# Performance work log

Hardware: AMD Instinct MI355X
Metric: run time of the kernel (lower is better)

The kernel has to match this reference:

```python
import jax, jax.numpy as jnp
import numpy as np

def setup_inputs() -> dict:
    key = jax.random.key(0)
    inputs_embeds = jax.random.normal(key, (16, 8192, 256), dtype=jnp.float32)
    return {"inputs_embeds": inputs_embeds}

def reference(inputs_embeds):
    # cumulative prefix mean along seq dim: mean over [:i+1] = cumsum / (i+1)
    S = inputs_embeds.shape[1]
    csum = jnp.cumsum(inputs_embeds, axis=1)  # [B, S, D]
    denom = jnp.arange(1, S + 1, dtype=inputs_embeds.dtype)[None, :, None]
    return (csum / denom,)
```

## Files before the change

kernel.cpp:

```cpp
#include <hip/hip_runtime.h>

#define BB 16
#define SS 8192
#define DD 256
#define D4 (DD / 4)
#define NC 256
#define CL (SS / NC)
#define G  16

#define NBLK (BB * NC)
#define AGGA_OFF (64 * 1024)
#define AGG_BYTES (NBLK * DD * 4)
#define AGGI_OFF (AGGA_OFF + AGG_BYTES)
#define WS_NEEDED ((size_t)(AGGI_OFF + AGG_BYTES))

typedef float nat4 __attribute__((ext_vector_type(4)));

union F2U { float2 f; unsigned long long u; };

__global__ __launch_bounds__(256) void avgseq_init(int* __restrict__ flags) {
    const int i = blockIdx.x * 256 + threadIdx.x;
    if (i < NBLK) flags[i] = 0;
}

__global__ __launch_bounds__(64, 4) void avgseq_lookback(
    const float4* __restrict__ x, float4* __restrict__ out,
    int* __restrict__ flags, unsigned long long* __restrict__ aggA,
    unsigned long long* __restrict__ aggI)
{
    const int blk = blockIdx.x;
    const int b = blk >> 8;
    const int c = blk & (NC - 1);
    const int t = threadIdx.x;

    const size_t base = ((size_t)b * SS + (size_t)c * CL) * D4 + t;
    const float4* p = x + base;

    float4 agg = make_float4(0.f, 0.f, 0.f, 0.f);
    for (int s0 = 0; s0 < CL; s0 += G) {
        float4 v[G];
#pragma unroll
        for (int g = 0; g < G; ++g) v[g] = p[(size_t)(s0 + g) * D4];
#pragma unroll
        for (int g = 0; g < G; ++g) {
            agg.x += v[g].x; agg.y += v[g].y; agg.z += v[g].z; agg.w += v[g].w;
        }
    }

    const size_t slot = (size_t)blk * (DD / 2) + (size_t)t * 2;

    if (c > 0) {
        F2U lo, hi;
        lo.f = make_float2(agg.x, agg.y);
        hi.f = make_float2(agg.z, agg.w);
        __hip_atomic_store(&aggA[slot],     lo.u, __ATOMIC_RELAXED, __HIP_MEMORY_SCOPE_AGENT);
        __hip_atomic_store(&aggA[slot + 1], hi.u, __ATOMIC_RELAXED, __HIP_MEMORY_SCOPE_AGENT);
        asm volatile("s_waitcnt vmcnt(0)" ::: "memory");
        __hip_atomic_store(&flags[blk], 1, __ATOMIC_RELAXED, __HIP_MEMORY_SCOPE_AGENT);
    }

    double rx = 0.0, ry = 0.0, rz = 0.0, rw = 0.0;
    if (c > 0) {
        int cc = c - 1;
        for (;;) {
            const int fblk = (b << 8) + cc;
            int f;
            for (;;) {
                f = __hip_atomic_load(&flags[fblk], __ATOMIC_RELAXED, __HIP_MEMORY_SCOPE_AGENT);
                f = __builtin_amdgcn_readfirstlane(f);
                if (f != 0) break;
                __builtin_amdgcn_s_sleep(1);
            }
            const unsigned long long* src = (f == 2) ? aggI : aggA;
            const size_t s2 = (size_t)fblk * (DD / 2) + (size_t)t * 2;
            F2U a, bq;
            a.u  = __hip_atomic_load(&src[s2],     __ATOMIC_RELAXED, __HIP_MEMORY_SCOPE_AGENT);
            bq.u = __hip_atomic_load(&src[s2 + 1], __ATOMIC_RELAXED, __HIP_MEMORY_SCOPE_AGENT);
            rx += a.f.x; ry += a.f.y; rz += bq.f.x; rw += bq.f.y;
            if (f == 2) break;
            --cc;
        }
    }
    const float4 run = make_float4((float)rx, (float)ry, (float)rz, (float)rw);

    if (c < NC - 1) {
        F2U lo, hi;
        lo.f = make_float2(run.x + agg.x, run.y + agg.y);
        hi.f = make_float2(run.z + agg.z, run.w + agg.w);
        __hip_atomic_store(&aggI[slot],     lo.u, __ATOMIC_RELAXED, __HIP_MEMORY_SCOPE_AGENT);
        __hip_atomic_store(&aggI[slot + 1], hi.u, __ATOMIC_RELAXED, __HIP_MEMORY_SCOPE_AGENT);
        asm volatile("s_waitcnt vmcnt(0)" ::: "memory");
        __hip_atomic_store(&flags[blk], 2, __ATOMIC_RELAXED, __HIP_MEMORY_SCOPE_AGENT);
    }

    float4 acc = run;
    float4* o = out + base;
    const int sb = c * CL;
    for (int s0 = 0; s0 < CL; s0 += G) {
        float4 v[G];
#pragma unroll
        for (int g = 0; g < G; ++g) v[g] = p[(size_t)(s0 + g) * D4];
#pragma unroll
        for (int g = 0; g < G; ++g) {
            acc.x += v[g].x; acc.y += v[g].y; acc.z += v[g].z; acc.w += v[g].w;
            const float r = __builtin_amdgcn_rcpf((float)(sb + s0 + g + 1));
            v[g] = make_float4(acc.x * r, acc.y * r, acc.z * r, acc.w * r);
        }
#pragma unroll
        for (int g = 0; g < G; ++g) {
            nat4 nv = { v[g].x, v[g].y, v[g].z, v[g].w };
            __builtin_nontemporal_store(nv, (nat4*)&o[(size_t)(s0 + g) * D4]);
        }
    }
}

__global__ __launch_bounds__(64) void avgseq_chunksum(const float4* __restrict__ x,
                                                      float4* __restrict__ ws) {
    const int blk = blockIdx.x;
    const int b = blk >> 8;
    const int c = blk & (NC - 1);
    const int t = threadIdx.x;
    const float4* p = x + ((size_t)b * SS + (size_t)c * CL) * D4 + t;
    float4 acc = make_float4(0.f, 0.f, 0.f, 0.f);
    for (int s0 = 0; s0 < CL; s0 += G) {
        float4 v[G];
#pragma unroll
        for (int g = 0; g < G; ++g) v[g] = p[(size_t)(s0 + g) * D4];
#pragma unroll
        for (int g = 0; g < G; ++g) {
            acc.x += v[g].x; acc.y += v[g].y; acc.z += v[g].z; acc.w += v[g].w;
        }
    }
    ws[((size_t)b * NC + c) * D4 + t] = acc;
}

__global__ __launch_bounds__(64) void avgseq_scanws(float4* __restrict__ ws) {
    const int b = blockIdx.x;
    const int t = threadIdx.x;
    float4* w = ws + (size_t)b * NC * D4 + t;
    float4 run = make_float4(0.f, 0.f, 0.f, 0.f);
#pragma unroll 8
    for (int c = 0; c < NC; ++c) {
        float4 v = w[(size_t)c * D4];
        w[(size_t)c * D4] = run;
        run.x += v.x; run.y += v.y; run.z += v.z; run.w += v.w;
    }
}

__global__ __launch_bounds__(64) void avgseq_scan(const float4* __restrict__ x,
                                                  const float4* __restrict__ ws,
                                                  float4* __restrict__ out) {
    const int blk = blockIdx.x;
    const int b = blk >> 8;
    const int c = blk & (NC - 1);
    const int t = threadIdx.x;
    float4 acc = ws[((size_t)b * NC + c) * D4 + t];
    const size_t base = ((size_t)b * SS + (size_t)c * CL) * D4 + t;
    const float4* p = x + base;
    float4* o = out + base;
    const int s0 = c * CL;
    for (int ss = 0; ss < CL; ss += G) {
        float4 v[G];
#pragma unroll
        for (int g = 0; g < G; ++g) v[g] = p[(size_t)(ss + g) * D4];
#pragma unroll
        for (int g = 0; g < G; ++g) {
            acc.x += v[g].x; acc.y += v[g].y; acc.z += v[g].z; acc.w += v[g].w;
            const float r = __builtin_amdgcn_rcpf((float)(s0 + ss + g + 1));
            v[g] = make_float4(acc.x * r, acc.y * r, acc.z * r, acc.w * r);
        }
#pragma unroll
        for (int g = 0; g < G; ++g) o[(size_t)(ss + g) * D4] = v[g];
    }
}

extern "C" void kernel_launch(void* const* d_in, const int* in_sizes, int n_in,
                              void* d_out, int out_size, void* d_ws, size_t ws_size,
                              hipStream_t stream) {
    const float4* x = (const float4*)d_in[0];
    float4* out = (float4*)d_out;

    if (ws_size >= WS_NEEDED) {
        int* flags = (int*)d_ws;
        unsigned long long* aggA = (unsigned long long*)((char*)d_ws + AGGA_OFF);
        unsigned long long* aggI = (unsigned long long*)((char*)d_ws + AGGI_OFF);
        avgseq_init<<<(NBLK + 255) / 256, 256, 0, stream>>>(flags);
        avgseq_lookback<<<NBLK, 64, 0, stream>>>(x, out, flags, aggA, aggI);
    } else {
        float4* ws = (float4*)d_ws;
        avgseq_chunksum<<<NBLK, 64, 0, stream>>>(x, ws);
        avgseq_scanws<<<BB, 64, 0, stream>>>(ws);
        avgseq_scan<<<NBLK, 64, 0, stream>>>(x, ws, out);
    }
}
```

Measured before the change: 272.1 us.

## Replace decoupled lookback with windowed summation of all predecessor aggregates

Removes the inclusive-prefix publication stage so each block only publishes its local chunk aggregate, then sums all preceding aggregates by polling flags and loading aggregates in windows of eight. This eliminates the serial chain where each block waits on its predecessor's inclusive prefix. In exchange each block reads up to 255 aggregate vectors, giving quadratic aggregate traffic and longer lookback for late chunks.

```diff
diff --git a/kernel.cpp b/kernel.cpp
--- a/kernel.cpp
+++ b/kernel.cpp
@@ -7,12 +7,12 @@
 #define NC 256
 #define CL (SS / NC)
 #define G  16
+#define W  8
 
 #define NBLK (BB * NC)
 #define AGGA_OFF (64 * 1024)
 #define AGG_BYTES (NBLK * DD * 4)
-#define AGGI_OFF (AGGA_OFF + AGG_BYTES)
-#define WS_NEEDED ((size_t)(AGGI_OFF + AGG_BYTES))
+#define WS_NEEDED ((size_t)(AGGA_OFF + AGG_BYTES))
 
 typedef float nat4 __attribute__((ext_vector_type(4)));
 
@@ -25,8 +25,7 @@
 
 __global__ __launch_bounds__(64, 4) void avgseq_lookback(
     const float4* __restrict__ x, float4* __restrict__ out,
-    int* __restrict__ flags, unsigned long long* __restrict__ aggA,
-    unsigned long long* __restrict__ aggI)
+    int* __restrict__ flags, unsigned long long* __restrict__ aggA)
 {
     const int blk = blockIdx.x;
     const int b = blk >> 8;
@@ -47,9 +46,8 @@
         }
     }
 
-    const size_t slot = (size_t)blk * (DD / 2) + (size_t)t * 2;
-
-    if (c > 0) {
+    if (c < NC - 1) {
+        const size_t slot = (size_t)blk * (DD / 2) + (size_t)t * 2;
         F2U lo, hi;
         lo.f = make_float2(agg.x, agg.y);
         hi.f = make_float2(agg.z, agg.w);
@@ -60,40 +58,40 @@
     }
 
     double rx = 0.0, ry = 0.0, rz = 0.0, rw = 0.0;
-    if (c > 0) {
+    {
+        const int fbase = b << 8;
         int cc = c - 1;
-        for (;;) {
-            const int fblk = (b << 8) + cc;
-            int f;
-            for (;;) {
-                f = __hip_atomic_load(&flags[fblk], __ATOMIC_RELAXED, __HIP_MEMORY_SCOPE_AGENT);
-                f = __builtin_amdgcn_readfirstlane(f);
-                if (f != 0) break;
+        while (cc >= 0) {
+            const int w = (cc >= W - 1) ? W : (cc + 1);
+            int f = 1;
+            if (t < w) f = __hip_atomic_load(&flags[fbase + cc - t],
+                                             __ATOMIC_RELAXED, __HIP_MEMORY_SCOPE_AGENT);
+            while (__ballot(f != 0) != ~0ULL) {
                 __builtin_amdgcn_s_sleep(1);
+                if (t < w) f = __hip_atomic_load(&flags[fbase + cc - t],
+                                                 __ATOMIC_RELAXED, __HIP_MEMORY_SCOPE_AGENT);
             }
-            const unsigned long long* src = (f == 2) ? aggI : aggA;
-            const size_t s2 = (size_t)fblk * (DD / 2) + (size_t)t * 2;
-            F2U a, bq;
-            a.u  = __hip_atomic_load(&src[s2],     __ATOMIC_RELAXED, __HIP_MEMORY_SCOPE_AGENT);
-            bq.u = __hip_atomic_load(&src[s2 + 1], __ATOMIC_RELAXED, __HIP_MEMORY_SCOPE_AGENT);
-            rx += a.f.x; ry += a.f.y; rz += bq.f.x; rw += bq.f.y;
-            if (f == 2) break;
-            --cc;
+            unsigned long long a0[W], a1[W];
+#pragma unroll
+            for (int k = 0; k < W; ++k) {
+                if (k < w) {
+                    const size_t s2 = (size_t)(fbase + cc - k) * (DD / 2) + (size_t)t * 2;
+                    a0[k] = __hip_atomic_load(&aggA[s2],     __ATOMIC_RELAXED, __HIP_MEMORY_SCOPE_AGENT);
+                    a1[k] = __hip_atomic_load(&aggA[s2 + 1], __ATOMIC_RELAXED, __HIP_MEMORY_SCOPE_AGENT);
+                }
+            }
+#pragma unroll
+            for (int k = 0; k < W; ++k) {
+                if (k < w) {
+                    F2U a, bq; a.u = a0[k]; bq.u = a1[k];
+                    rx += a.f.x; ry += a.f.y; rz += bq.f.x; rw += bq.f.y;
+                }
+            }
+            cc -= w;
         }
     }
-    const float4 run = make_float4((float)rx, (float)ry, (float)rz, (float)rw);
+    float4 acc = make_float4((float)rx, (float)ry, (float)rz, (float)rw);
 
-    if (c < NC - 1) {
-        F2U lo, hi;
-        lo.f = make_float2(run.x + agg.x, run.y + agg.y);
-        hi.f = make_float2(run.z + agg.z, run.w + agg.w);
-        __hip_atomic_store(&aggI[slot],     lo.u, __ATOMIC_RELAXED, __HIP_MEMORY_SCOPE_AGENT);
-        __hip_atomic_store(&aggI[slot + 1], hi.u, __ATOMIC_RELAXED, __HIP_MEMORY_SCOPE_AGENT);
-        asm volatile("s_waitcnt vmcnt(0)" ::: "memory");
-        __hip_atomic_store(&flags[blk], 2, __ATOMIC_RELAXED, __HIP_MEMORY_SCOPE_AGENT);
-    }
-
-    float4 acc = run;
     float4* o = out + base;
     const int sb = c * CL;
     for (int s0 = 0; s0 < CL; s0 += G) {
@@ -183,9 +181,8 @@
     if (ws_size >= WS_NEEDED) {
         int* flags = (int*)d_ws;
         unsigned long long* aggA = (unsigned long long*)((char*)d_ws + AGGA_OFF);
-        unsigned long long* aggI = (unsigned long long*)((char*)d_ws + AGGI_OFF);
         avgseq_init<<<(NBLK + 255) / 256, 256, 0, stream>>>(flags);
-        avgseq_lookback<<<NBLK, 64, 0, stream>>>(x, out, flags, aggA, aggI);
+        avgseq_lookback<<<NBLK, 64, 0, stream>>>(x, out, flags, aggA);
     } else {
         float4* ws = (float4*)d_ws;
         avgseq_chunksum<<<NBLK, 64, 0, stream>>>(x, ws);
```

Result: slower. 316.9 us (+16.5%).
